# Performance work log

Measured on AMD Instinct MI355X. Metric: run time of the kernel, lower is better.

Reference implementation:

```python
import jax, jax.numpy as jnp
import numpy as np

N = 50000      # nodes
E = 800000     # edges (avg degree 16)
D = 64         # emb_dim
L = 5          # num_layer
BN_EPS = 1e-5


def setup_inputs() -> dict:
    key = jax.random.key(0)
    ks = jax.random.split(key, 10)
    x = jax.random.randint(ks[0], (N,), 0, 1)                      # indices into 1-row embedding
    edge_index = jax.random.randint(ks[1], (2, E), 0, N)
    edge_attr = jax.random.normal(ks[2], (E, 7), dtype=jnp.float32)
    s = lambda k, shape: (jax.random.normal(k, shape, dtype=jnp.float32) * 0.05)
    node_emb = s(ks[3], (1, D))
    # per-layer GINConv params, stacked on a leading layer axis for lax.scan
    We = s(ks[4], (L, 7, D));   be = jnp.zeros((L, D), jnp.float32)      # edge_encoder
    eps = jnp.zeros((L,), jnp.float32)                                   # GIN eps
    W1 = s(ks[5], (L, D, 2 * D)); b1 = jnp.zeros((L, 2 * D), jnp.float32)  # mlp linear1
    g1 = jnp.ones((L, 2 * D), jnp.float32); bb1 = jnp.zeros((L, 2 * D), jnp.float32)  # mlp BN
    W2 = s(ks[6], (L, 2 * D, D)); b2 = jnp.zeros((L, D), jnp.float32)    # mlp linear2
    g2 = jnp.ones((L, D), jnp.float32); bb2 = jnp.zeros((L, D), jnp.float32)  # outer BN
    return dict(x=x, edge_index=edge_index, edge_attr=edge_attr, node_emb=node_emb,
                We=We, be=be, eps=eps, W1=W1, b1=b1, g1=g1, bb1=bb1,
                W2=W2, b2=b2, g2=g2, bb2=bb2)


def _bn(a, g, b):
    # BatchNorm1d in training mode: batch statistics over node axis, biased var
    m = a.mean(axis=0)
    v = jnp.var(a, axis=0)
    return (a - m) * jax.lax.rsqrt(v + BN_EPS) * g + b


def reference(x, edge_index, edge_attr, node_emb, We, be, eps,
              W1, b1, g1, bb1, W2, b2, g2, bb2):
    src, dst = edge_index[0], edge_index[1]
    h = node_emb[x]                                    # [N, D]
    relu_flags = jnp.arange(L) < (L - 1)               # ReLU on all but last layer

    def step(h, p):
        We_, be_, eps_, W1_, b1_, g1_, bb1_, W2_, b2_, g2_, bb2_, flag = p
        ee = edge_attr @ We_ + be_                     # [E, D] edge embeddings
        msg = jax.nn.relu(h[src] + ee)                 # gather + elementwise
        agg = jax.ops.segment_sum(msg, dst, num_segments=N)  # scatter-add
        z = (1.0 + eps_) * h + agg                     # GIN combine
        a = jax.nn.relu(_bn(z @ W1_ + b1_, g1_, bb1_)) # mlp: lin -> BN -> ReLU
        hb = _bn(a @ W2_ + b2_, g2_, bb2_)             # lin -> outer BN
        h_new = jnp.where(flag, jax.nn.relu(hb), hb)   # dropout omitted (eval)
        return h_new, None

    h, _ = jax.lax.scan(step, h, (We, be, eps, W1, b1, g1, bb1, W2, b2, g2, bb2, relu_flags))
    return h                                           # JK='last'
```

## Files before the change

kernel.cpp:

```cpp
#include <hip/hip_runtime.h>
#include <hip/hip_fp16.h>

#define NN 50000
#define EE 800000
#define NB 782
#define NBKT 196
#define BCAP 4608

typedef _Float16 f16x8 __attribute__((ext_vector_type(8)));
typedef _Float16 f16x2 __attribute__((ext_vector_type(2)));
typedef float f32x4 __attribute__((ext_vector_type(4)));

__device__ __forceinline__ unsigned h2u(__half2 h) {
    union { __half2 h; unsigned u; } c; c.h = h; return c.u;
}
__device__ __forceinline__ f16x2 u2h(unsigned u) {
    union { unsigned u; f16x2 h; } c; c.u = u; return c.h;
}

__global__ __launch_bounds__(256) void bin_kernel(
    const int* __restrict__ ei, const float* __restrict__ ea,
    int* __restrict__ bktcur, int4* __restrict__ srec,
    unsigned short* __restrict__ sdst)
{
    __shared__ int cnt[NBKT], base[NBKT];
    const int t = threadIdx.x;
    if (t < NBKT) cnt[t] = 0;
    __syncthreads();
    const int e0 = blockIdx.x << 12;
    int meta[16];
#pragma unroll
    for (int j = 0; j < 16; ++j) {
        const int e = e0 + (j << 8) + t;
        if (e < EE) {
            const int d = ei[EE + e];
            const int bk = d >> 8;
            const int rk = atomicAdd(&cnt[bk], 1);
            meta[j] = (rk << 16) | (bk << 8) | (d & 255);
        } else meta[j] = -1;
    }
    __syncthreads();
    if (t < NBKT) base[t] = cnt[t] ? atomicAdd(&bktcur[t], cnt[t]) : 0;
    __syncthreads();
#pragma unroll
    for (int j = 0; j < 16; ++j) {
        if (meta[j] < 0) continue;
        const int bk = (meta[j] >> 8) & 255;
        const int slot = base[bk] + (meta[j] >> 16);
        if (slot >= BCAP) continue;
        const int pos = bk * BCAP + slot;
        const int e = e0 + (j << 8) + t;
        const int src = ei[e];
        const float* a = ea + e * 7;
        const unsigned h0 = __half_as_ushort(__float2half(a[0]));
        const unsigned h1 = __half_as_ushort(__float2half(a[1]));
        const unsigned h2 = __half_as_ushort(__float2half(a[2]));
        const unsigned h3 = __half_as_ushort(__float2half(a[3]));
        const unsigned h4 = __half_as_ushort(__float2half(a[4]));
        const unsigned h5 = __half_as_ushort(__float2half(a[5]));
        const unsigned h6 = __half_as_ushort(__float2half(a[6]));
        srec[pos] = make_int4((int)(h0 | (h1 << 16)), (int)(h2 | (h3 << 16)),
                              (int)(h4 | (h5 << 16)), (int)(h6 | ((unsigned)src << 16)));
        sdst[pos] = (unsigned short)(meta[j] & 255);
    }
}

__global__ __launch_bounds__(256) void bcountA_kernel(
    const int* __restrict__ bktcur, const unsigned short* __restrict__ sdst,
    int* __restrict__ deg, int* __restrict__ bsum)
{
    __shared__ int nc[256], sm[256];
    const int b = blockIdx.x, t = threadIdx.x;
    nc[t] = 0;
    __syncthreads();
    const int nE = min(bktcur[b], BCAP);
    const int sb = b * BCAP;
    for (int i = t; i < nE; i += 256) atomicAdd(&nc[(int)sdst[sb + i]], 1);
    __syncthreads();
    const int node = (b << 8) + t;
    if (node < NN) deg[node] = nc[t];
    sm[t] = (node < NN) ? ((nc[t] + 7) & ~7) : 0;
    __syncthreads();
    for (int o = 128; o > 0; o >>= 1) {
        if (t < o) sm[t] += sm[t + o];
        __syncthreads();
    }
    if (t == 0) bsum[b] = sm[0];
}

__global__ __launch_bounds__(256) void scanB_kernel(int* __restrict__ bsum) {
    __shared__ int sm[256];
    const int t = threadIdx.x;
    const int v = (t < 196) ? bsum[t] : 0;
    sm[t] = v;
    __syncthreads();
    for (int o = 1; o < 256; o <<= 1) {
        const int u = (t >= o) ? sm[t - o] : 0;
        __syncthreads();
        sm[t] += u;
        __syncthreads();
    }
    bsum[t] = sm[t] - v;
}

__global__ __launch_bounds__(256) void scanC_kernel(const int* __restrict__ deg,
                                                    const int* __restrict__ bsum,
                                                    int* __restrict__ off) {
    __shared__ int sm[256];
    const int t = threadIdx.x;
    const int i = (blockIdx.x << 8) + t;
    const int v = (i < NN) ? ((deg[i] + 7) & ~7) : 0;
    sm[t] = v;
    __syncthreads();
    for (int o = 1; o < 256; o <<= 1) {
        const int u = (t >= o) ? sm[t - o] : 0;
        __syncthreads();
        sm[t] += u;
        __syncthreads();
    }
    const int excl = bsum[blockIdx.x] + sm[t] - v;
    if (i < NN) off[i] = excl;
    else if (i == NN) off[NN] = excl;
}

__global__ __launch_bounds__(256) void place2_kernel(
    const int* __restrict__ bktcur, const int* __restrict__ off,
    const int4* __restrict__ srec, const unsigned short* __restrict__ sdst,
    int4* __restrict__ pea)
{
    __shared__ int curs[256];
    const int b = blockIdx.x, t = threadIdx.x;
    const int node = (b << 8) + t;
    curs[t] = (node < NN) ? off[node] : 0;
    __syncthreads();
    const int nE = min(bktcur[b], BCAP);
    const int sb = b * BCAP;
    for (int i = t; i < nE; i += 256) {
        const int ln = (int)sdst[sb + i];
        const int p = atomicAdd(&curs[ln], 1);
        pea[p] = srec[sb + i];
    }
    __syncthreads();
    if (node < NN) {
        const int end = off[node + 1];
        for (int p = curs[t]; p < end; ++p)
            pea[p] = make_int4(0, 0, 0, (int)(((unsigned)NN) << 16));
    }
}

__global__ __launch_bounds__(256) void wprep_kernel(
    const float* __restrict__ W1, const float* __restrict__ W2,
    const float* __restrict__ We, const float* __restrict__ be,
    _Float16* __restrict__ W1s, _Float16* __restrict__ W2s,
    unsigned* __restrict__ Wepk, unsigned* __restrict__ be2)
{
    const int i = (blockIdx.x << 8) + threadIdx.x;
    if (i < 40960) {
        const int l = i >> 13, j = i & 8191, k = j >> 7, n = j & 127;
        W1s[(l << 13) + ((((k >> 3) << 7) + n) << 3) + (k & 7)] = (_Float16)W1[i];
    } else if (i < 81920) {
        const int i2 = i - 40960;
        const int l = i2 >> 13, j = i2 & 8191, k = j >> 6, n = j & 63;
        W2s[(l << 13) + ((((k >> 3) << 6) + n) << 3) + (k & 7)] = (_Float16)W2[i2];
    } else if (i < 83040) {
        const int i3 = i - 81920;
        const int l = i3 / 224;
        const int r = i3 - l * 224;
        const int k = r >> 5, s = r & 31;
        const float* W = We + l * 448 + (k << 6) + (s << 1);
        Wepk[i3] = h2u(__floats2half2_rn(W[0], W[1]));
    } else if (i < 83200) {
        const int i4 = i - 83040;
        const int l = i4 >> 5, s = i4 & 31;
        const float* B = be + (l << 6) + (s << 1);
        be2[i4] = h2u(__floats2half2_rn(B[0], B[1]));
    }
}

__global__ __launch_bounds__(256) void hprep_kernel(
    const float* __restrict__ y2, const float* __restrict__ acc2,
    const float* __restrict__ g2p, const float* __restrict__ bb2p,
    __half* __restrict__ h16)
{
    __shared__ float scshL[128];
    const int t = threadIdx.x;
    if (t < 64) {
        float ss = 0.f, qq = 0.f;
#pragma unroll
        for (int c = 0; c < 8; ++c) {
            ss += acc2[(c << 7) + t];
            qq += acc2[(c << 7) + 64 + t];
        }
        const float m = ss * (1.0f / NN);
        const float v = fmaxf(qq * (1.0f / NN) - m * m, 0.0f);
        const float sc = g2p[t] * rsqrtf(v + 1e-5f);
        scshL[t] = sc;
        scshL[64 + t] = bb2p[t] - m * sc;
    }
    __syncthreads();
    const int i4 = (blockIdx.x << 8) + t;
    const float4 v = ((const float4*)y2)[i4];
    const int d0 = (i4 << 2) & 63;
    const float a = fmaxf(fmaf(v.x, scshL[d0 + 0], scshL[64 + d0 + 0]), 0.f);
    const float b = fmaxf(fmaf(v.y, scshL[d0 + 1], scshL[64 + d0 + 1]), 0.f);
    const float c = fmaxf(fmaf(v.z, scshL[d0 + 2], scshL[64 + d0 + 2]), 0.f);
    const float d = fmaxf(fmaf(v.w, scshL[d0 + 3], scshL[64 + d0 + 3]), 0.f);
    *(int2*)(h16 + (i4 << 2)) =
        make_int2((int)h2u(__floats2half2_rn(a, b)),
                  (int)h2u(__floats2half2_rn(c, d)));
}

__global__ __launch_bounds__(256) void hprep0_kernel(
    const int* __restrict__ x, const float* __restrict__ nemb,
    __half* __restrict__ h16, unsigned* __restrict__ z32)
{
    const int i4 = (blockIdx.x << 8) + threadIdx.x;
    if (blockIdx.x == 0 && threadIdx.x < 32)
        ((unsigned*)h16)[(NN << 5) + threadIdx.x] = 0xFBFFFBFFu;
    if (i4 < 1536) z32[1600000 + i4] = 0u;
    const int n = i4 >> 4;
    const float4 v = ((const float4*)nemb)[(x[n] << 4) + (i4 & 15)];
    *(int2*)(h16 + (i4 << 2)) =
        make_int2((int)h2u(__floats2half2_rn(v.x, v.y)),
                  (int)h2u(__floats2half2_rn(v.z, v.w)));
}

__global__ __launch_bounds__(256) void gather_kernel(
    const int* __restrict__ off, const int4* __restrict__ pea,
    const unsigned* __restrict__ h32,
    const unsigned* __restrict__ Wepk, const unsigned* __restrict__ be2,
    const float* __restrict__ epsp,
    unsigned* __restrict__ z32)
{
    const int t = threadIdx.x;
    const int lane = t & 63;
    const int s = lane & 31;
    const int n = (blockIdx.x << 3) + ((t >> 6) << 1) + (lane >> 5);

    const f16x2 w0 = u2h(Wepk[s]),       w1 = u2h(Wepk[32 + s]),
                w2 = u2h(Wepk[64 + s]),  w3 = u2h(Wepk[96 + s]),
                w4 = u2h(Wepk[128 + s]), w5 = u2h(Wepk[160 + s]),
                w6 = u2h(Wepk[192 + s]);
    const f16x2 beh = u2h(be2[s]);

    const int e0 = off[n], e1 = off[n + 1];

    f16x2 acc2 = (f16x2){(_Float16)0.f, (_Float16)0.f};
    for (int e = e0; e < e1; e += 8) {
        int4 pk[8];
#pragma unroll
        for (int j = 0; j < 8; ++j) pk[j] = pea[e + j];
        unsigned hv[8];
#pragma unroll
        for (int j = 0; j < 8; ++j) {
            const int src = (int)(((unsigned)pk[j].w) >> 16);
            hv[j] = h32[(src << 5) + s];
        }
#pragma unroll
        for (int j = 0; j < 8; ++j) {
            const f16x2 a01 = u2h((unsigned)pk[j].x);
            const f16x2 a23 = u2h((unsigned)pk[j].y);
            const f16x2 a45 = u2h((unsigned)pk[j].z);
            const f16x2 a6x = u2h((unsigned)pk[j].w);
            f16x2 ee = beh;
            ee += (f16x2){a01[0], a01[0]} * w0;
            ee += (f16x2){a01[1], a01[1]} * w1;
            ee += (f16x2){a23[0], a23[0]} * w2;
            ee += (f16x2){a23[1], a23[1]} * w3;
            ee += (f16x2){a45[0], a45[0]} * w4;
            ee += (f16x2){a45[1], a45[1]} * w5;
            ee += (f16x2){a6x[0], a6x[0]} * w6;
            f16x2 m2 = u2h(hv[j]) + ee;
            const _Float16 zz = (_Float16)0.f;
            m2 = (f16x2){ m2[0] > zz ? m2[0] : zz, m2[1] > zz ? m2[1] : zz };
            acc2 += m2;
        }
    }
    const f16x2 hn2 = u2h(h32[(n << 5) + s]);
    const float e1f = 1.0f + epsp[0];
    const float zLo = fmaf(e1f, (float)hn2[0], (float)acc2[0]);
    const float zHi = fmaf(e1f, (float)hn2[1], (float)acc2[1]);
    z32[(n << 5) + s] = h2u(__floats2half2_rn(zLo, zHi));
}

__global__ __launch_bounds__(256) void mm1_kernel(
    const _Float16* __restrict__ z16, const _Float16* __restrict__ W1s,
    const float* __restrict__ b1p, _Float16* __restrict__ y1h,
    float* __restrict__ acc1)
{
    __shared__ float smS[4][128], smQ[4][128];
    const int t = threadIdx.x;
    const int wv = t >> 6, lane = t & 63;
    const int q = lane >> 4, ln = lane & 15;
    const int r0 = blockIdx.x << 6;

    const int rowm = r0 + (wv << 4) + ln;
    const f16x8 af0 = *(const f16x8*)(z16 + rowm * 64 + (q << 3));
    const f16x8 af1 = *(const f16x8*)(z16 + rowm * 64 + 32 + (q << 3));

    f32x4 acc[8];
#pragma unroll
    for (int n0 = 0; n0 < 8; ++n0) acc[n0] = (f32x4){0.f, 0.f, 0.f, 0.f};
#pragma unroll
    for (int n0 = 0; n0 < 8; ++n0) {
        const f16x8 bf0 = *(const f16x8*)(W1s + (((q << 7) + (n0 << 4) + ln) << 3));
        const f16x8 bf1 = *(const f16x8*)(W1s + ((((4 + q) << 7) + (n0 << 4) + ln) << 3));
        acc[n0] = __builtin_amdgcn_mfma_f32_16x16x32_f16(af0, bf0, acc[n0], 0, 0, 0);
        acc[n0] = __builtin_amdgcn_mfma_f32_16x16x32_f16(af1, bf1, acc[n0], 0, 0, 0);
    }

    const int baseRow = r0 + (wv << 4) + (q << 2);
#pragma unroll
    for (int n0 = 0; n0 < 8; ++n0) {
        const int col = (n0 << 4) + ln;
        const float bb = b1p[col];
        float s = 0.f, sq = 0.f;
#pragma unroll
        for (int rg = 0; rg < 4; ++rg) {
            const int row = baseRow + rg;
            const float y = acc[n0][rg] + bb;
            y1h[row * 128 + col] = (_Float16)y;
            const float m = (row < NN) ? 1.f : 0.f;
            s = fmaf(m, y, s); sq = fmaf(m, y * y, sq);
        }
        s += __shfl_xor(s, 16); s += __shfl_xor(s, 32);
        sq += __shfl_xor(sq, 16); sq += __shfl_xor(sq, 32);
        if (lane < 16) { smS[wv][col] = s; smQ[wv][col] = sq; }
    }
    __syncthreads();
    if (t < 128) {
        const float s4 = smS[0][t] + smS[1][t] + smS[2][t] + smS[3][t];
        const float q4 = smQ[0][t] + smQ[1][t] + smQ[2][t] + smQ[3][t];
        float* a1 = acc1 + ((blockIdx.x & 7) << 8);
        atomicAdd(&a1[t], s4);
        atomicAdd(&a1[128 + t], q4);
    }
}

__global__ __launch_bounds__(256) void mm2_kernel(
    const _Float16* __restrict__ y1h, const float* __restrict__ acc1,
    const float* __restrict__ g1p, const float* __restrict__ bb1p,
    const _Float16* __restrict__ W2s, const float* __restrict__ b2,
    float* __restrict__ y2, float* __restrict__ acc2)
{
    __shared__ float smS[4][64], smQ[4][64];
    __shared__ float scshL[256];
    const int t = threadIdx.x;
    const int wv = t >> 6, lane = t & 63;
    const int q = lane >> 4, ln = lane & 15;
    const int r0 = blockIdx.x << 6;

    if (t < 128) {
        float ss = 0.f, qq = 0.f;
#pragma unroll
        for (int c = 0; c < 8; ++c) {
            ss += acc1[(c << 8) + t];
            qq += acc1[(c << 8) + 128 + t];
        }
        const float m = ss * (1.0f / NN);
        const float v = fmaxf(qq * (1.0f / NN) - m * m, 0.0f);
        const float sc = g1p[t] * rsqrtf(v + 1e-5f);
        scshL[t] = sc;
        scshL[128 + t] = bb1p[t] - m * sc;
    }
    __syncthreads();

    const int rowm = r0 + (wv << 4) + ln;
    f16x8 af[4];
#pragma unroll
    for (int ks = 0; ks < 4; ++ks) {
        const int k0 = (ks << 5) + (q << 3);
        const f16x8 raw = *(const f16x8*)(y1h + rowm * 128 + k0);
        f16x8 a;
#pragma unroll
        for (int j = 0; j < 8; ++j) {
            const float sc = scshL[k0 + j], sh = scshL[128 + k0 + j];
            a[j] = (_Float16)fmaxf(fmaf((float)raw[j], sc, sh), 0.f);
        }
        af[ks] = a;
    }

    f32x4 acc[4];
#pragma unroll
    for (int n0 = 0; n0 < 4; ++n0) acc[n0] = (f32x4){0.f, 0.f, 0.f, 0.f};
#pragma unroll
    for (int n0 = 0; n0 < 4; ++n0) {
#pragma unroll
        for (int ks = 0; ks < 4; ++ks) {
            const f16x8 bf = *(const f16x8*)(
                W2s + (((((ks << 2) + q) << 6) + (n0 << 4) + ln) << 3));
            acc[n0] = __builtin_amdgcn_mfma_f32_16x16x32_f16(af[ks], bf, acc[n0], 0, 0, 0);
        }
    }

    const int baseRow = r0 + (wv << 4) + (q << 2);
#pragma unroll
    for (int n0 = 0; n0 < 4; ++n0) {
        const int col = (n0 << 4) + ln;
        const float bb = b2[col];
        float s = 0.f, sq = 0.f;
#pragma unroll
        for (int rg = 0; rg < 4; ++rg) {
            const int row = baseRow + rg;
            const float y = acc[n0][rg] + bb;
            y2[row * 64 + col] = y;
            const float m = (row < NN) ? 1.f : 0.f;
            s = fmaf(m, y, s); sq = fmaf(m, y * y, sq);
        }
        s += __shfl_xor(s, 16); s += __shfl_xor(s, 32);
        sq += __shfl_xor(sq, 16); sq += __shfl_xor(sq, 32);
        if (lane < 16) { smS[wv][col] = s; smQ[wv][col] = sq; }
    }
    __syncthreads();
    if (t < 64) {
        const float s4 = smS[0][t] + smS[1][t] + smS[2][t] + smS[3][t];
        const float q4 = smQ[0][t] + smQ[1][t] + smQ[2][t] + smQ[3][t];
        float* a2 = acc2 + ((blockIdx.x & 7) << 7);
        atomicAdd(&a2[t], s4);
        atomicAdd(&a2[64 + t], q4);
    }
}

__global__ __launch_bounds__(256) void final_kernel(
    const float* __restrict__ y2, const float* __restrict__ acc2,
    const float* __restrict__ g2p, const float* __restrict__ bb2p,
    float* __restrict__ out)
{
    __shared__ float scshL[128];
    const int t = threadIdx.x;
    if (t < 64) {
        float ss = 0.f, qq = 0.f;
#pragma unroll
        for (int c = 0; c < 8; ++c) {
            ss += acc2[(c << 7) + t];
            qq += acc2[(c << 7) + 64 + t];
        }
        const float m = ss * (1.0f / NN);
        const float v = fmaxf(qq * (1.0f / NN) - m * m, 0.0f);
        const float sc = g2p[t] * rsqrtf(v + 1e-5f);
        scshL[t] = sc;
        scshL[64 + t] = bb2p[t] - m * sc;
    }
    __syncthreads();
    const int i4 = (blockIdx.x << 8) + t;
    const float4 v = ((const float4*)y2)[i4];
    const int d0 = (i4 << 2) & 63;
    float4 o;
    o.x = fmaf(v.x, scshL[d0 + 0], scshL[64 + d0 + 0]);
    o.y = fmaf(v.y, scshL[d0 + 1], scshL[64 + d0 + 1]);
    o.z = fmaf(v.z, scshL[d0 + 2], scshL[64 + d0 + 2]);
    o.w = fmaf(v.w, scshL[d0 + 3], scshL[64 + d0 + 3]);
    ((float4*)out)[i4] = o;
}

extern "C" void kernel_launch(void* const* d_in, const int* in_sizes, int n_in,
                              void* d_out, int out_size, void* d_ws, size_t ws_size,
                              hipStream_t stream)
{
    const int*   x    = (const int*)d_in[0];
    const int*   ei   = (const int*)d_in[1];
    const float* ea   = (const float*)d_in[2];
    const float* nemb = (const float*)d_in[3];
    const float* We   = (const float*)d_in[4];
    const float* be   = (const float*)d_in[5];
    const float* eps  = (const float*)d_in[6];
    const float* W1   = (const float*)d_in[7];
    const float* b1   = (const float*)d_in[8];
    const float* g1   = (const float*)d_in[9];
    const float* bb1  = (const float*)d_in[10];
    const float* W2   = (const float*)d_in[11];
    const float* b2   = (const float*)d_in[12];
    const float* g2   = (const float*)d_in[13];
    const float* bb2  = (const float*)d_in[14];
    float* out = (float*)d_out;

    int*      iws   = (int*)d_ws;
    float*    fws   = (float*)d_ws;
    int*      off   = iws + 0;
    int*      deg   = iws + 50048;
    int*      bsum  = iws + 150144;
    int*      bktcur= iws + 150784;
    float*    accbuf= fws + 151040;
    _Float16* W1s   = (_Float16*)(fws + 451072);
    _Float16* W2s   = (_Float16*)(fws + 471552);
    unsigned* Wepk  = (unsigned*)(fws + 492032);
    unsigned* be2   = (unsigned*)(fws + 493152);
    int4*     pea   = (int4*)(iws + 493312);
    _Float16* z16   = (_Float16*)(fws + 5093312);
    _Float16* y1h   = (_Float16*)(fws + 6694848);
    float*    y2    = fws + 6694848;
    __half*   h16   = (__half*)(fws + 9897920);

    int4*           srec = (int4*)(fws + 5093312);
    unsigned short* sdst = (unsigned short*)(fws + 9897920);

    hipMemsetAsync(bktcur, 0, (166400 - 150784) * sizeof(int), stream);

    bin_kernel    <<<196,  256, 0, stream>>>(ei, ea, bktcur, srec, sdst);
    bcountA_kernel<<<NBKT, 256, 0, stream>>>(bktcur, sdst, deg, bsum);
    scanB_kernel  <<<1,    256, 0, stream>>>(bsum);
    scanC_kernel  <<<196,  256, 0, stream>>>(deg, bsum, off);
    place2_kernel <<<NBKT, 256, 0, stream>>>(bktcur, off, srec, sdst, pea);
    wprep_kernel  <<<325,  256, 0, stream>>>(W1, W2, We, be, W1s, W2s, Wepk, be2);
    hprep0_kernel <<<3125, 256, 0, stream>>>(x, nemb, h16, (unsigned*)z16);

    for (int l = 0; l < 5; ++l) {
        float* acc1 = accbuf + l * 3072;
        float* acc2 = accbuf + l * 3072 + 2048;

        gather_kernel<<<6250, 256, 0, stream>>>(
            off, pea, (const unsigned*)h16, Wepk + l * 224, be2 + l * 32,
            eps + l, (unsigned*)z16);

        mm1_kernel<<<NB, 256, 0, stream>>>(z16, W1s + l * 8192, b1 + l * 128,
                                           y1h, acc1);

        mm2_kernel<<<NB, 256, 0, stream>>>(y1h, acc1, g1 + l * 128, bb1 + l * 128,
                                           W2s + l * 8192, b2 + l * 64, y2, acc2);

        if (l < 4)
            hprep_kernel<<<3125, 256, 0, stream>>>(y2, acc2, g2 + l * 64,
                                                   bb2 + l * 64, h16);
    }

    final_kernel<<<3125, 256, 0, stream>>>(y2, accbuf + 4 * 3072 + 2048,
                                           g2 + 4 * 64, bb2 + 4 * 64, out);
}
```

Measured before the change: 420.4 us.

## Fuse edge gather-aggregate into first MLP matmul via shared-memory z tile

Merges the per-node edge gather/aggregate kernel with the first linear layer. Each block now computes its 64 rows of z into a swizzled LDS tile and feeds MFMA directly, removing the z16 global write/read round trip and one launch per layer. In exchange the grid drops from 6250 to 782 blocks, so each block does 8 sequential gather passes, which lowers parallelism and latency hiding for the irregular gather. Padding rows past N are now zeroed in-kernel instead of by hprep0.

```diff
diff --git a/kernel.cpp b/kernel.cpp
--- a/kernel.cpp
+++ b/kernel.cpp
@@ -212,12 +212,11 @@
 
 __global__ __launch_bounds__(256) void hprep0_kernel(
     const int* __restrict__ x, const float* __restrict__ nemb,
-    __half* __restrict__ h16, unsigned* __restrict__ z32)
+    __half* __restrict__ h16)
 {
     const int i4 = (blockIdx.x << 8) + threadIdx.x;
     if (blockIdx.x == 0 && threadIdx.x < 32)
         ((unsigned*)h16)[(NN << 5) + threadIdx.x] = 0xFBFFFBFFu;
-    if (i4 < 1536) z32[1600000 + i4] = 0u;
     const int n = i4 >> 4;
     const float4 v = ((const float4*)nemb)[(x[n] << 4) + (i4 & 15)];
     *(int2*)(h16 + (i4 << 2)) =
@@ -225,78 +224,82 @@
                   (int)h2u(__floats2half2_rn(v.z, v.w)));
 }
 
-__global__ __launch_bounds__(256) void gather_kernel(
+__global__ __launch_bounds__(256) void gmm1_kernel(
     const int* __restrict__ off, const int4* __restrict__ pea,
     const unsigned* __restrict__ h32,
     const unsigned* __restrict__ Wepk, const unsigned* __restrict__ be2,
     const float* __restrict__ epsp,
-    unsigned* __restrict__ z32)
-{
-    const int t = threadIdx.x;
-    const int lane = t & 63;
-    const int s = lane & 31;
-    const int n = (blockIdx.x << 3) + ((t >> 6) << 1) + (lane >> 5);
-
-    const f16x2 w0 = u2h(Wepk[s]),       w1 = u2h(Wepk[32 + s]),
-                w2 = u2h(Wepk[64 + s]),  w3 = u2h(Wepk[96 + s]),
-                w4 = u2h(Wepk[128 + s]), w5 = u2h(Wepk[160 + s]),
-                w6 = u2h(Wepk[192 + s]);
-    const f16x2 beh = u2h(be2[s]);
-
-    const int e0 = off[n], e1 = off[n + 1];
-
-    f16x2 acc2 = (f16x2){(_Float16)0.f, (_Float16)0.f};
-    for (int e = e0; e < e1; e += 8) {
-        int4 pk[8];
-#pragma unroll
-        for (int j = 0; j < 8; ++j) pk[j] = pea[e + j];
-        unsigned hv[8];
-#pragma unroll
-        for (int j = 0; j < 8; ++j) {
-            const int src = (int)(((unsigned)pk[j].w) >> 16);
-            hv[j] = h32[(src << 5) + s];
-        }
-#pragma unroll
-        for (int j = 0; j < 8; ++j) {
-            const f16x2 a01 = u2h((unsigned)pk[j].x);
-            const f16x2 a23 = u2h((unsigned)pk[j].y);
-            const f16x2 a45 = u2h((unsigned)pk[j].z);
-            const f16x2 a6x = u2h((unsigned)pk[j].w);
-            f16x2 ee = beh;
-            ee += (f16x2){a01[0], a01[0]} * w0;
-            ee += (f16x2){a01[1], a01[1]} * w1;
-            ee += (f16x2){a23[0], a23[0]} * w2;
-            ee += (f16x2){a23[1], a23[1]} * w3;
-            ee += (f16x2){a45[0], a45[0]} * w4;
-            ee += (f16x2){a45[1], a45[1]} * w5;
-            ee += (f16x2){a6x[0], a6x[0]} * w6;
-            f16x2 m2 = u2h(hv[j]) + ee;
-            const _Float16 zz = (_Float16)0.f;
-            m2 = (f16x2){ m2[0] > zz ? m2[0] : zz, m2[1] > zz ? m2[1] : zz };
-            acc2 += m2;
-        }
-    }
-    const f16x2 hn2 = u2h(h32[(n << 5) + s]);
-    const float e1f = 1.0f + epsp[0];
-    const float zLo = fmaf(e1f, (float)hn2[0], (float)acc2[0]);
-    const float zHi = fmaf(e1f, (float)hn2[1], (float)acc2[1]);
-    z32[(n << 5) + s] = h2u(__floats2half2_rn(zLo, zHi));
-}
-
-__global__ __launch_bounds__(256) void mm1_kernel(
-    const _Float16* __restrict__ z16, const _Float16* __restrict__ W1s,
-    const float* __restrict__ b1p, _Float16* __restrict__ y1h,
-    float* __restrict__ acc1)
-{
+    const _Float16* __restrict__ W1s, const float* __restrict__ b1p,
+    _Float16* __restrict__ y1h, float* __restrict__ acc1)
+{
+    __shared__ unsigned zl[64][32];
     __shared__ float smS[4][128], smQ[4][128];
     const int t = threadIdx.x;
     const int wv = t >> 6, lane = t & 63;
     const int q = lane >> 4, ln = lane & 15;
+    const int s = lane & 31, half = lane >> 5;
     const int r0 = blockIdx.x << 6;
 
-    const int rowm = r0 + (wv << 4) + ln;
-    const f16x8 af0 = *(const f16x8*)(z16 + rowm * 64 + (q << 3));
-    const f16x8 af1 = *(const f16x8*)(z16 + rowm * 64 + 32 + (q << 3));
+    {
+        const f16x2 w0 = u2h(Wepk[s]),       w1 = u2h(Wepk[32 + s]),
+                    w2 = u2h(Wepk[64 + s]),  w3 = u2h(Wepk[96 + s]),
+                    w4 = u2h(Wepk[128 + s]), w5 = u2h(Wepk[160 + s]),
+                    w6 = u2h(Wepk[192 + s]);
+        const f16x2 beh = u2h(be2[s]);
+        const float e1f = 1.0f + epsp[0];
+        for (int pass = 0; pass < 8; ++pass) {
+            const int lr = (pass << 3) + (wv << 1) + half;
+            const int n = r0 + lr;
+            unsigned zv = 0u;
+            if (n < NN) {
+                const int eb0 = off[n], eb1 = off[n + 1];
+                f16x2 acc2 = (f16x2){(_Float16)0.f, (_Float16)0.f};
+                for (int e = eb0; e < eb1; e += 8) {
+                    int4 pk[8];
+#pragma unroll
+                    for (int j = 0; j < 8; ++j) pk[j] = pea[e + j];
+                    unsigned hv[8];
+#pragma unroll
+                    for (int j = 0; j < 8; ++j) {
+                        const int src = (int)(((unsigned)pk[j].w) >> 16);
+                        hv[j] = h32[(src << 5) + s];
+                    }
+#pragma unroll
+                    for (int j = 0; j < 8; ++j) {
+                        const f16x2 a01 = u2h((unsigned)pk[j].x);
+                        const f16x2 a23 = u2h((unsigned)pk[j].y);
+                        const f16x2 a45 = u2h((unsigned)pk[j].z);
+                        const f16x2 a6x = u2h((unsigned)pk[j].w);
+                        f16x2 ee = beh;
+                        ee += (f16x2){a01[0], a01[0]} * w0;
+                        ee += (f16x2){a01[1], a01[1]} * w1;
+                        ee += (f16x2){a23[0], a23[0]} * w2;
+                        ee += (f16x2){a23[1], a23[1]} * w3;
+                        ee += (f16x2){a45[0], a45[0]} * w4;
+                        ee += (f16x2){a45[1], a45[1]} * w5;
+                        ee += (f16x2){a6x[0], a6x[0]} * w6;
+                        f16x2 m2 = u2h(hv[j]) + ee;
+                        const _Float16 zz = (_Float16)0.f;
+                        m2 = (f16x2){ m2[0] > zz ? m2[0] : zz,
+                                      m2[1] > zz ? m2[1] : zz };
+                        acc2 += m2;
+                    }
+                }
+                const f16x2 hn2 = u2h(h32[(n << 5) + s]);
+                const float zLo = fmaf(e1f, (float)hn2[0], (float)acc2[0]);
+                const float zHi = fmaf(e1f, (float)hn2[1], (float)acc2[1]);
+                zv = h2u(__floats2half2_rn(zLo, zHi));
+            }
+            zl[lr][s ^ ((lr & 7) << 2)] = zv;
+        }
+    }
+    __syncthreads();
+
+    const int rowml = (wv << 4) + ln;
+    const int rsw = rowml & 7;
+    const unsigned* zrow = &zl[rowml][0];
+    const f16x8 af0 = *(const f16x8*)(zrow + ((q ^ rsw) << 2));
+    const f16x8 af1 = *(const f16x8*)(zrow + (((4 + q) ^ rsw) << 2));
 
     f32x4 acc[8];
 #pragma unroll
@@ -314,18 +317,18 @@
     for (int n0 = 0; n0 < 8; ++n0) {
         const int col = (n0 << 4) + ln;
         const float bb = b1p[col];
-        float s = 0.f, sq = 0.f;
+        float sa = 0.f, sq = 0.f;
 #pragma unroll
         for (int rg = 0; rg < 4; ++rg) {
             const int row = baseRow + rg;
             const float y = acc[n0][rg] + bb;
             y1h[row * 128 + col] = (_Float16)y;
             const float m = (row < NN) ? 1.f : 0.f;
-            s = fmaf(m, y, s); sq = fmaf(m, y * y, sq);
-        }
-        s += __shfl_xor(s, 16); s += __shfl_xor(s, 32);
+            sa = fmaf(m, y, sa); sq = fmaf(m, y * y, sq);
+        }
+        sa += __shfl_xor(sa, 16); sa += __shfl_xor(sa, 32);
         sq += __shfl_xor(sq, 16); sq += __shfl_xor(sq, 32);
-        if (lane < 16) { smS[wv][col] = s; smQ[wv][col] = sq; }
+        if (lane < 16) { smS[wv][col] = sa; smQ[wv][col] = sq; }
     }
     __syncthreads();
     if (t < 128) {
@@ -398,18 +401,18 @@
     for (int n0 = 0; n0 < 4; ++n0) {
         const int col = (n0 << 4) + ln;
         const float bb = b2[col];
-        float s = 0.f, sq = 0.f;
+        float sa = 0.f, sq = 0.f;
 #pragma unroll
         for (int rg = 0; rg < 4; ++rg) {
             const int row = baseRow + rg;
             const float y = acc[n0][rg] + bb;
             y2[row * 64 + col] = y;
             const float m = (row < NN) ? 1.f : 0.f;
-            s = fmaf(m, y, s); sq = fmaf(m, y * y, sq);
-        }
-        s += __shfl_xor(s, 16); s += __shfl_xor(s, 32);
+            sa = fmaf(m, y, sa); sq = fmaf(m, y * y, sq);
+        }
+        sa += __shfl_xor(sa, 16); sa += __shfl_xor(sa, 32);
         sq += __shfl_xor(sq, 16); sq += __shfl_xor(sq, 32);
-        if (lane < 16) { smS[wv][col] = s; smQ[wv][col] = sq; }
+        if (lane < 16) { smS[wv][col] = sa; smQ[wv][col] = sq; }
     }
     __syncthreads();
     if (t < 64) {
@@ -486,7 +489,6 @@
     unsigned* Wepk  = (unsigned*)(fws + 492032);
     unsigned* be2   = (unsigned*)(fws + 493152);
     int4*     pea   = (int4*)(iws + 493312);
-    _Float16* z16   = (_Float16*)(fws + 5093312);
     _Float16* y1h   = (_Float16*)(fws + 6694848);
     float*    y2    = fws + 6694848;
     __half*   h16   = (__half*)(fws + 9897920);
@@ -502,18 +504,15 @@
     scanC_kernel  <<<196,  256, 0, stream>>>(deg, bsum, off);
     place2_kernel <<<NBKT, 256, 0, stream>>>(bktcur, off, srec, sdst, pea);
     wprep_kernel  <<<325,  256, 0, stream>>>(W1, W2, We, be, W1s, W2s, Wepk, be2);
-    hprep0_kernel <<<3125, 256, 0, stream>>>(x, nemb, h16, (unsigned*)z16);
+    hprep0_kernel <<<3125, 256, 0, stream>>>(x, nemb, h16);
 
     for (int l = 0; l < 5; ++l) {
         float* acc1 = accbuf + l * 3072;
         float* acc2 = accbuf + l * 3072 + 2048;
 
-        gather_kernel<<<6250, 256, 0, stream>>>(
+        gmm1_kernel<<<NB, 256, 0, stream>>>(
             off, pea, (const unsigned*)h16, Wepk + l * 224, be2 + l * 32,
-            eps + l, (unsigned*)z16);
-
-        mm1_kernel<<<NB, 256, 0, stream>>>(z16, W1s + l * 8192, b1 + l * 128,
-                                           y1h, acc1);
+            eps + l, W1s + l * 8192, b1 + l * 128, y1h, acc1);
 
         mm2_kernel<<<NB, 256, 0, stream>>>(y1h, acc1, g1 + l * 128, bb1 + l * 128,
                                            W2s + l * 8192, b2 + l * 64, y2, acc2);
```

Result: slower. 443.9 us (+5.6%).

## Split each node's edge gather across two half-wavefronts and fuse setup kernels

Applied to the files above, without the earlier changes.

The gather kernel now assigns one wavefront per node instead of two nodes per wavefront. Each half-wave processes alternating 8-edge chunks, and the partial sums are combined with a cross-half shuffle, so the grid size doubles. This is meant to cut the per-node serial latency of high-degree nodes and raise memory-level parallelism, at the cost of idle lanes for low-degree nodes and an extra shuffle. Separately, the two-level scan is merged into one kernel that redundantly rescans block sums, and the weight-prep and h-prep kernels are fused into one launch to remove two launches.

```diff
diff --git a/kernel.cpp b/kernel.cpp
--- a/kernel.cpp
+++ b/kernel.cpp
@@ -16,6 +16,9 @@
 }
 __device__ __forceinline__ f16x2 u2h(unsigned u) {
     union { unsigned u; f16x2 h; } c; c.u = u; return c.h;
+}
+__device__ __forceinline__ unsigned f2u(f16x2 h) {
+    union { f16x2 h; unsigned u; } c; c.h = h; return c.u;
 }
 
 __global__ __launch_bounds__(256) void bin_kernel(
@@ -88,10 +91,22 @@
     if (t == 0) bsum[b] = sm[0];
 }
 
-__global__ __launch_bounds__(256) void scanB_kernel(int* __restrict__ bsum) {
-    __shared__ int sm[256];
-    const int t = threadIdx.x;
-    const int v = (t < 196) ? bsum[t] : 0;
+__global__ __launch_bounds__(256) void scanC_kernel(const int* __restrict__ deg,
+                                                    const int* __restrict__ bsum,
+                                                    int* __restrict__ off) {
+    __shared__ int sm[256], bs[256], bsr[256];
+    const int t = threadIdx.x;
+    const int bv = (t < NBKT) ? bsum[t] : 0;
+    bs[t] = bv; bsr[t] = bv;
+    __syncthreads();
+    for (int o = 1; o < 256; o <<= 1) {
+        const int u = (t >= o) ? bs[t - o] : 0;
+        __syncthreads();
+        bs[t] += u;
+        __syncthreads();
+    }
+    const int i = (blockIdx.x << 8) + t;
+    const int v = (i < NN) ? ((deg[i] + 7) & ~7) : 0;
     sm[t] = v;
     __syncthreads();
     for (int o = 1; o < 256; o <<= 1) {
@@ -100,25 +115,8 @@
         sm[t] += u;
         __syncthreads();
     }
-    bsum[t] = sm[t] - v;
-}
-
-__global__ __launch_bounds__(256) void scanC_kernel(const int* __restrict__ deg,
-                                                    const int* __restrict__ bsum,
-                                                    int* __restrict__ off) {
-    __shared__ int sm[256];
-    const int t = threadIdx.x;
-    const int i = (blockIdx.x << 8) + t;
-    const int v = (i < NN) ? ((deg[i] + 7) & ~7) : 0;
-    sm[t] = v;
-    __syncthreads();
-    for (int o = 1; o < 256; o <<= 1) {
-        const int u = (t >= o) ? sm[t - o] : 0;
-        __syncthreads();
-        sm[t] += u;
-        __syncthreads();
-    }
-    const int excl = bsum[blockIdx.x] + sm[t] - v;
+    const int gbase = bs[blockIdx.x] - bsr[blockIdx.x];
+    const int excl = gbase + sm[t] - v;
     if (i < NN) off[i] = excl;
     else if (i == NN) off[NN] = excl;
 }
@@ -148,13 +146,27 @@
     }
 }
 
-__global__ __launch_bounds__(256) void wprep_kernel(
+__global__ __launch_bounds__(256) void prep_kernel(
+    const int* __restrict__ x, const float* __restrict__ nemb,
+    __half* __restrict__ h16, unsigned* __restrict__ z32,
     const float* __restrict__ W1, const float* __restrict__ W2,
     const float* __restrict__ We, const float* __restrict__ be,
     _Float16* __restrict__ W1s, _Float16* __restrict__ W2s,
     unsigned* __restrict__ Wepk, unsigned* __restrict__ be2)
 {
-    const int i = (blockIdx.x << 8) + threadIdx.x;
+    if (blockIdx.x < 3125) {
+        const int i4 = (blockIdx.x << 8) + threadIdx.x;
+        if (blockIdx.x == 0 && threadIdx.x < 32)
+            ((unsigned*)h16)[(NN << 5) + threadIdx.x] = 0xFBFFFBFFu;
+        if (i4 < 1536) z32[1600000 + i4] = 0u;
+        const int n = i4 >> 4;
+        const float4 v = ((const float4*)nemb)[(x[n] << 4) + (i4 & 15)];
+        *(int2*)(h16 + (i4 << 2)) =
+            make_int2((int)h2u(__floats2half2_rn(v.x, v.y)),
+                      (int)h2u(__floats2half2_rn(v.z, v.w)));
+        return;
+    }
+    const int i = ((blockIdx.x - 3125) << 8) + threadIdx.x;
     if (i < 40960) {
         const int l = i >> 13, j = i & 8191, k = j >> 7, n = j & 127;
         W1s[(l << 13) + ((((k >> 3) << 7) + n) << 3) + (k & 7)] = (_Float16)W1[i];
@@ -210,21 +222,6 @@
                   (int)h2u(__floats2half2_rn(c, d)));
 }
 
-__global__ __launch_bounds__(256) void hprep0_kernel(
-    const int* __restrict__ x, const float* __restrict__ nemb,
-    __half* __restrict__ h16, unsigned* __restrict__ z32)
-{
-    const int i4 = (blockIdx.x << 8) + threadIdx.x;
-    if (blockIdx.x == 0 && threadIdx.x < 32)
-        ((unsigned*)h16)[(NN << 5) + threadIdx.x] = 0xFBFFFBFFu;
-    if (i4 < 1536) z32[1600000 + i4] = 0u;
-    const int n = i4 >> 4;
-    const float4 v = ((const float4*)nemb)[(x[n] << 4) + (i4 & 15)];
-    *(int2*)(h16 + (i4 << 2)) =
-        make_int2((int)h2u(__floats2half2_rn(v.x, v.y)),
-                  (int)h2u(__floats2half2_rn(v.z, v.w)));
-}
-
 __global__ __launch_bounds__(256) void gather_kernel(
     const int* __restrict__ off, const int4* __restrict__ pea,
     const unsigned* __restrict__ h32,
@@ -235,7 +232,8 @@
     const int t = threadIdx.x;
     const int lane = t & 63;
     const int s = lane & 31;
-    const int n = (blockIdx.x << 3) + ((t >> 6) << 1) + (lane >> 5);
+    const int hh = lane >> 5;
+    const int n = (blockIdx.x << 2) + (t >> 6);
 
     const f16x2 w0 = u2h(Wepk[s]),       w1 = u2h(Wepk[32 + s]),
                 w2 = u2h(Wepk[64 + s]),  w3 = u2h(Wepk[96 + s]),
@@ -246,7 +244,7 @@
     const int e0 = off[n], e1 = off[n + 1];
 
     f16x2 acc2 = (f16x2){(_Float16)0.f, (_Float16)0.f};
-    for (int e = e0; e < e1; e += 8) {
+    for (int e = e0 + (hh << 3); e < e1; e += 16) {
         int4 pk[8];
 #pragma unroll
         for (int j = 0; j < 8; ++j) pk[j] = pea[e + j];
@@ -276,11 +274,14 @@
             acc2 += m2;
         }
     }
-    const f16x2 hn2 = u2h(h32[(n << 5) + s]);
-    const float e1f = 1.0f + epsp[0];
-    const float zLo = fmaf(e1f, (float)hn2[0], (float)acc2[0]);
-    const float zHi = fmaf(e1f, (float)hn2[1], (float)acc2[1]);
-    z32[(n << 5) + s] = h2u(__floats2half2_rn(zLo, zHi));
+    acc2 += u2h((unsigned)__shfl_xor((int)f2u(acc2), 32));
+    if (hh == 0) {
+        const f16x2 hn2 = u2h(h32[(n << 5) + s]);
+        const float e1f = 1.0f + epsp[0];
+        const float zLo = fmaf(e1f, (float)hn2[0], (float)acc2[0]);
+        const float zHi = fmaf(e1f, (float)hn2[1], (float)acc2[1]);
+        z32[(n << 5) + s] = h2u(__floats2half2_rn(zLo, zHi));
+    }
 }
 
 __global__ __launch_bounds__(256) void mm1_kernel(
@@ -398,18 +399,18 @@
     for (int n0 = 0; n0 < 4; ++n0) {
         const int col = (n0 << 4) + ln;
         const float bb = b2[col];
-        float s = 0.f, sq = 0.f;
+        float sa = 0.f, sq = 0.f;
 #pragma unroll
         for (int rg = 0; rg < 4; ++rg) {
             const int row = baseRow + rg;
             const float y = acc[n0][rg] + bb;
             y2[row * 64 + col] = y;
             const float m = (row < NN) ? 1.f : 0.f;
-            s = fmaf(m, y, s); sq = fmaf(m, y * y, sq);
-        }
-        s += __shfl_xor(s, 16); s += __shfl_xor(s, 32);
+            sa = fmaf(m, y, sa); sq = fmaf(m, y * y, sq);
+        }
+        sa += __shfl_xor(sa, 16); sa += __shfl_xor(sa, 32);
         sq += __shfl_xor(sq, 16); sq += __shfl_xor(sq, 32);
-        if (lane < 16) { smS[wv][col] = s; smQ[wv][col] = sq; }
+        if (lane < 16) { smS[wv][col] = sa; smQ[wv][col] = sq; }
     }
     __syncthreads();
     if (t < 64) {
@@ -498,17 +499,16 @@
 
     bin_kernel    <<<196,  256, 0, stream>>>(ei, ea, bktcur, srec, sdst);
     bcountA_kernel<<<NBKT, 256, 0, stream>>>(bktcur, sdst, deg, bsum);
-    scanB_kernel  <<<1,    256, 0, stream>>>(bsum);
     scanC_kernel  <<<196,  256, 0, stream>>>(deg, bsum, off);
     place2_kernel <<<NBKT, 256, 0, stream>>>(bktcur, off, srec, sdst, pea);
-    wprep_kernel  <<<325,  256, 0, stream>>>(W1, W2, We, be, W1s, W2s, Wepk, be2);
-    hprep0_kernel <<<3125, 256, 0, stream>>>(x, nemb, h16, (unsigned*)z16);
+    prep_kernel   <<<3450, 256, 0, stream>>>(x, nemb, h16, (unsigned*)z16,
+                                             W1, W2, We, be, W1s, W2s, Wepk, be2);
 
     for (int l = 0; l < 5; ++l) {
         float* acc1 = accbuf + l * 3072;
         float* acc2 = accbuf + l * 3072 + 2048;
 
-        gather_kernel<<<6250, 256, 0, stream>>>(
+        gather_kernel<<<12500, 256, 0, stream>>>(
             off, pea, (const unsigned*)h16, Wepk + l * 224, be2 + l * 32,
             eps + l, (unsigned*)z16);
 
```

Measured after the change: 434.1 us. +3.3%, slower.
